# Performance work log

Measured on AMD Instinct MI355X. Metric: run time of the kernel, lower is better.

The kernel has to match this reference:

```python
import jax, jax.numpy as jnp
import numpy as np

BANDWIDTH = 8.0  # gaussian kernel std


def setup_inputs() -> dict:
    key = jax.random.key(0)
    k1, k2 = jax.random.split(key)
    B, N, M, D = 2, 8192, 8192, 64
    return {
        "points": jax.random.normal(k1, (B, N, D), dtype=jnp.float32),
        "ref_points": jax.random.normal(k2, (B, M, D), dtype=jnp.float32),
    }


def reference(points, ref_points):
    # Squared pairwise distances via the |x|^2 + |y|^2 - 2<x,y> expansion
    # (same math as ((x_i - y_j)**2).sum(-1), avoids a [B,N,M,D] intermediate).
    sq_p = jnp.sum(points * points, axis=-1)          # [B,N]
    sq_r = jnp.sum(ref_points * ref_points, axis=-1)  # [B,M]
    s_ij = (sq_p[:, :, None] + sq_r[:, None, :]
            - 2.0 * jnp.einsum('bnd,bmd->bnm', points, ref_points))  # [B,N,M]
    # Gaussian kernel
    k_ij = jnp.exp(s_ij * (-1.0 / (2.0 * BANDWIDTH ** 2)))  # [B,N,M]
    # Weighted mean of reference points (nominator.sum(2) / k_ij.sum(2))
    nominator = jnp.einsum('bnm,bmd->bnd', k_ij, ref_points)  # [B,N,D]
    denominator = jnp.sum(k_ij, axis=-1, keepdims=True)       # [B,N,1]
    return nominator / denominator
```

## Files before the change

### kernel.cpp

```cpp
#include <hip/hip_runtime.h>

constexpr int B_ = 2, N_ = 8192, M_ = 8192, Dd = 64;
constexpr int TN = 128;
constexpr int TM = 64;
constexpr int SPLIT = 8;
constexpr int MCHUNK = M_ / SPLIT;
constexpr int NCHUNKS = MCHUNK / TM;
constexpr int NT = N_ / TN;
constexpr float LOG2E   = 1.4426950408889634f;
constexpr float SCALE_S = LOG2E / 64.0f;
constexpr float SCALE_N = -LOG2E / 128.0f;

using s16x8 = __attribute__((ext_vector_type(8))) short;
using f32x4 = __attribute__((ext_vector_type(4))) float;
using f32x2v = __attribute__((ext_vector_type(2))) float;
using bf16x2 = __attribute__((ext_vector_type(2))) __bf16;

#if defined(__has_builtin)
#if __has_builtin(__builtin_amdgcn_exp2f)
#define EXP2(x) __builtin_amdgcn_exp2f(x)
#endif
#endif
#ifndef EXP2
#define EXP2(x) exp2f(x)
#endif

__device__ __forceinline__ unsigned pk2(float lo, float hi) {
  f32x2v f;
  f[0] = lo;
  f[1] = hi;
  bf16x2 h = __builtin_convertvector(f, bf16x2);
  return __builtin_bit_cast(unsigned, h);
}
__device__ __forceinline__ f32x4 mfma16(s16x8 a, s16x8 b, f32x4 c) {
  return __builtin_amdgcn_mfma_f32_16x16x32_bf16(a, b, c, 0, 0, 0);
}
__device__ __forceinline__ float dot4(float4 f) {
  return f.x * f.x + f.y * f.y + f.z * f.z + f.w * f.w;
}


__global__ __launch_bounds__(256, 4) void msflash_kernel(
    const float* __restrict__ pts, const float* __restrict__ ref,
    float* __restrict__ num_acc, float* __restrict__ den_acc) {
  __shared__ unsigned short ldsY2[2][TM][72];
  __shared__ unsigned short ldsYT2[2][Dd][64];
  __shared__ unsigned short ldsQ[4][16][32];
  __shared__ float lds_bm2[2][TM];

  const int tid  = threadIdx.x;
  const int w    = tid >> 6;
  const int lane = tid & 63;
  const int l15  = lane & 15, quad = lane >> 4;
  const int ytsw = quad + (l15 & 7);
  const int psm  = l15 & 3;

  const int s  = blockIdx.x & (SPLIT - 1);
  const int r  = blockIdx.x >> 3;
  const int bb = r / NT;
  const int nt_ = r % NT;
  const int n0 = nt_ * TN;
  const int m_begin = s * MCHUNK;

  const int rowl_s = tid >> 2, q_s = tid & 3;
  const float* ybase = ref + ((size_t)bb * M_ + m_begin + rowl_s) * Dd + q_s * 16;
  float4 fv0, fv1, fv2, fv3;

  auto loadfv = [&](int cc) {
    const float* yp = ybase + (size_t)cc * TM * Dd;
    fv0 = ((const float4*)yp)[0];
    fv1 = ((const float4*)yp)[1];
    fv2 = ((const float4*)yp)[2];
    fv3 = ((const float4*)yp)[3];
  };
  auto stage = [&](int bp) {
    unsigned pkd[8] = {pk2(fv0.x, fv0.y), pk2(fv0.z, fv0.w),
                       pk2(fv1.x, fv1.y), pk2(fv1.z, fv1.w),
                       pk2(fv2.x, fv2.y), pk2(fv2.z, fv2.w),
                       pk2(fv3.x, fv3.y), pk2(fv3.z, fv3.w)};
    float sq = dot4(fv0) + dot4(fv1) + dot4(fv2) + dot4(fv3);
    sq += __shfl_xor(sq, 1);
    sq += __shfl_xor(sq, 2);
    if (q_s == 0) lds_bm2[bp][rowl_s] = sq * SCALE_N;
    uint4* dv = (uint4*)&ldsY2[bp][rowl_s][q_s * 16];
    dv[0] = make_uint4(pkd[0], pkd[1], pkd[2], pkd[3]);
    dv[1] = make_uint4(pkd[4], pkd[5], pkd[6], pkd[7]);
    const int tsw = (rowl_s >> 3) + 2 * q_s;
    const int mlo = rowl_s & 7;
#pragma unroll
    for (int j = 0; j < 8; j++) {
      const int d0 = q_s * 16 + 2 * j;
      const int c0 = (tsw + ((2 * j) & 7)) & 7;
      const int c1 = (tsw + ((2 * j + 1) & 7)) & 7;
      ldsYT2[bp][d0][(c0 << 3) + mlo]     = (unsigned short)pkd[j];
      ldsYT2[bp][d0 + 1][(c1 << 3) + mlo] = (unsigned short)(pkd[j] >> 16);
    }
  };

  loadfv(0);
  unsigned short (*ldsX)[72] = (unsigned short (*)[72]) & ldsY2[0][0][0];
  float* lds_an2 = (float*)&ldsQ[0][0][0];
  {
    const int rowl = tid >> 1, half = tid & 1;
    const float* gp = pts + ((size_t)bb * N_ + n0 + rowl) * Dd + half * 32;
    float sq = 0.f;
    unsigned pkd[16];
#pragma unroll
    for (int i = 0; i < 8; i++) {
      float4 f = ((const float4*)gp)[i];
      sq += dot4(f);
      pkd[2 * i + 0] = pk2(f.x, f.y);
      pkd[2 * i + 1] = pk2(f.z, f.w);
    }
    sq += __shfl_xor(sq, 1);
    if (half == 0) lds_an2[rowl] = sq * SCALE_N;
    uint4* dv = (uint4*)&ldsX[rowl][half * 32];
#pragma unroll
    for (int i = 0; i < 4; i++)
      dv[i] = make_uint4(pkd[4 * i], pkd[4 * i + 1], pkd[4 * i + 2], pkd[4 * i + 3]);
  }
  __syncthreads();

  s16x8 bx[2][2];
  float anr_s[2];
#pragma unroll
  for (int rt = 0; rt < 2; rt++) {
#pragma unroll
    for (int ks = 0; ks < 2; ks++)
      bx[rt][ks] = *(const s16x8*)&ldsX[w * 32 + rt * 16 + l15][ks * 32 + quad * 8];
    anr_s[rt] = lds_an2[w * 32 + rt * 16 + l15];
  }
  __syncthreads();

  stage(0);
  loadfv(1);
  __syncthreads();

  f32x4 o[2][4], den[2];
#pragma unroll
  for (int rt = 0; rt < 2; rt++) {
    den[rt] = f32x4{0.f, 0.f, 0.f, 0.f};
#pragma unroll
    for (int dt = 0; dt < 4; dt++) o[rt][dt] = f32x4{0.f, 0.f, 0.f, 0.f};
  }
  s16x8 ones;
#pragma unroll
  for (int j = 0; j < 8; j++) ones[j] = (l15 == 0) ? (short)0x3F80 : (short)0;

  int p = 0;
  for (int c = 0; c < NCHUNKS; ++c) {
    f32x4 sf[2][4];
#pragma unroll
    for (int ct = 0; ct < 4; ct++) {
      s16x8 a0 = *(const s16x8*)&ldsY2[p][ct * 16 + l15][quad * 8];
      s16x8 a1 = *(const s16x8*)&ldsY2[p][ct * 16 + l15][32 + quad * 8];
#pragma unroll
      for (int rt = 0; rt < 2; rt++) {
        f32x4 acc = f32x4{0.f, 0.f, 0.f, 0.f};
        acc = mfma16(a0, bx[rt][0], acc);
        acc = mfma16(a1, bx[rt][1], acc);
        sf[rt][ct] = acc;
      }
    }
#pragma unroll
    for (int ks = 0; ks < 2; ks++) {
      f32x4 bmA = *(const f32x4*)&lds_bm2[p][(2 * ks + 0) * 16 + quad * 4];
      f32x4 bmB = *(const f32x4*)&lds_bm2[p][(2 * ks + 1) * 16 + quad * 4];
      s16x8 pf01[2];
#pragma unroll
      for (int rt = 0; rt < 2; rt++) {
#pragma unroll
        for (int cl = 0; cl < 2; cl++) {
          const f32x4& bm = cl ? bmB : bmA;
          const f32x4& sv = sf[rt][2 * ks + cl];
          float e0 = EXP2(sv[0] * SCALE_S + (anr_s[rt] + bm[0]));
          float e1 = EXP2(sv[1] * SCALE_S + (anr_s[rt] + bm[1]));
          float e2 = EXP2(sv[2] * SCALE_S + (anr_s[rt] + bm[2]));
          float e3 = EXP2(sv[3] * SCALE_S + (anr_s[rt] + bm[3]));
          const int ch = ((2 * cl + (quad >> 1)) ^ psm);
          *(uint2*)&ldsQ[w][l15][ch * 8 + (quad & 1) * 4] =
              make_uint2(pk2(e0, e1), pk2(e2, e3));
        }
        pf01[rt] = *(const s16x8*)&ldsQ[w][l15][(quad ^ psm) * 8];
      }
#pragma unroll
      for (int dt = 0; dt < 4; dt++) {
        const unsigned short* yt = &ldsYT2[p][dt * 16 + l15][0];
        s16x8 a = *(const s16x8*)&yt[((ytsw + 4 * ks + 2 * dt) & 7) << 3];
        o[0][dt] = mfma16(a, pf01[0], o[0][dt]);
        o[1][dt] = mfma16(a, pf01[1], o[1][dt]);
      }
      den[0] = mfma16(ones, pf01[0], den[0]);
      den[1] = mfma16(ones, pf01[1], den[1]);
    }
    stage(p ^ 1);
    loadfv(c + 2 < NCHUNKS ? c + 2 : NCHUNKS - 1);
    __syncthreads();
    p ^= 1;
  }

  float* ldsO = (float*)&ldsY2[0][0][0] + (size_t)w * 1152;
  float* nb = num_acc + ((size_t)bb * N_ + n0) * Dd;
#pragma unroll
  for (int rt = 0; rt < 2; rt++) {
#pragma unroll
    for (int dt = 0; dt < 4; dt++) {
      const int base = l15 * 66 + dt * 16 + quad * 4;
      *(float2*)&ldsO[base + 0] = make_float2(o[rt][dt][0], o[rt][dt][1]);
      *(float2*)&ldsO[base + 2] = make_float2(o[rt][dt][2], o[rt][dt][3]);
    }
    const int nrow = w * 32 + rt * 16;
#pragma unroll
    for (int rr = 0; rr < 16; rr++) {
      float v = ldsO[rr * 66 + lane];
      atomicAdd(&nb[(size_t)(nrow + rr) * Dd + lane], v);
    }
    if (quad == 0)
      atomicAdd(&den_acc[(size_t)bb * N_ + n0 + nrow + l15], den[rt][0]);
  }
}

__global__ __launch_bounds__(256) void msdiv_kernel(
    const float* __restrict__ num, const float* __restrict__ den,
    float* __restrict__ out) {
  const int i = blockIdx.x * 256 + threadIdx.x;
  float4 v = ((const float4*)num)[i];
  const float inv = 1.0f / den[i >> 4];
  ((float4*)out)[i] = make_float4(v.x * inv, v.y * inv, v.z * inv, v.w * inv);
}

extern "C" void kernel_launch(void* const* d_in, const int* in_sizes, int n_in,
                              void* d_out, int out_size, void* d_ws, size_t ws_size,
                              hipStream_t stream) {
  const float* pts = (const float*)d_in[0];
  const float* ref = (const float*)d_in[1];
  float* out = (float*)d_out;
  float* num = (float*)d_ws;
  float* den = num + (size_t)B_ * N_ * Dd;
  const size_t acc_bytes = ((size_t)B_ * N_ * Dd + (size_t)B_ * N_) * sizeof(float);

  hipMemsetAsync(d_ws, 0, acc_bytes, stream);
  msflash_kernel<<<dim3(B_ * NT * SPLIT), dim3(256), 0, stream>>>(pts, ref, num, den);
  const int tot4 = B_ * N_ * Dd / 4;
  msdiv_kernel<<<dim3(tot4 / 256), dim3(256), 0, stream>>>(num, den, out);
}
```

Before: 157.0 us.

## Switch flash mean-shift kernel to 32x32x16 MFMA with register-shuffled P fragments

Replaces the 16x16x32 bf16 MFMA tiling with 32x32x16 MFMA, so each wave computes its 32-row tile with fewer, larger matrix ops. The exp outputs are regrouped into the B-operand layout with a cross-half lane shuffle instead of a round trip through per-wave LDS scratch. The denominator is summed in scalar registers instead of by an extra ones-vector MFMA. The double-buffered LDS staging with register prefetch is dropped for a single buffer with two barriers per chunk. That cuts LDS use and may raise occupancy, but global load latency is no longer overlapped with compute.

```diff
diff --git a/kernel.cpp b/kernel.cpp
--- a/kernel.cpp
+++ b/kernel.cpp
@@ -11,8 +11,8 @@
 constexpr float SCALE_S = LOG2E / 64.0f;
 constexpr float SCALE_N = -LOG2E / 128.0f;
 
-using s16x8 = __attribute__((ext_vector_type(8))) short;
-using f32x4 = __attribute__((ext_vector_type(4))) float;
+using s16x8  = __attribute__((ext_vector_type(8))) short;
+using f32x16 = __attribute__((ext_vector_type(16))) float;
 using f32x2v = __attribute__((ext_vector_type(2))) float;
 using bf16x2 = __attribute__((ext_vector_type(2))) __bf16;
 
@@ -32,8 +32,8 @@
   bf16x2 h = __builtin_convertvector(f, bf16x2);
   return __builtin_bit_cast(unsigned, h);
 }
-__device__ __forceinline__ f32x4 mfma16(s16x8 a, s16x8 b, f32x4 c) {
-  return __builtin_amdgcn_mfma_f32_16x16x32_bf16(a, b, c, 0, 0, 0);
+__device__ __forceinline__ f32x16 mfma32(s16x8 a, s16x8 b, f32x16 c) {
+  return __builtin_amdgcn_mfma_f32_32x32x16_bf16(a, b, c, 0, 0, 0);
 }
 __device__ __forceinline__ float dot4(float4 f) {
   return f.x * f.x + f.y * f.y + f.z * f.z + f.w * f.w;
@@ -43,17 +43,17 @@
 __global__ __launch_bounds__(256, 4) void msflash_kernel(
     const float* __restrict__ pts, const float* __restrict__ ref,
     float* __restrict__ num_acc, float* __restrict__ den_acc) {
-  __shared__ unsigned short ldsY2[2][TM][72];
-  __shared__ unsigned short ldsYT2[2][Dd][64];
-  __shared__ unsigned short ldsQ[4][16][32];
-  __shared__ float lds_bm2[2][TM];
+  __shared__ __align__(16) unsigned char smem[18944];
+  unsigned short (*ldsY)[72]  = (unsigned short (*)[72])  smem;
+  unsigned short (*ldsYT)[64] = (unsigned short (*)[64]) (smem + 9216);
+  float* bm2 = (float*)(smem + 17408);
+  float* an2 = (float*)(smem + 18432);
 
   const int tid  = threadIdx.x;
   const int w    = tid >> 6;
   const int lane = tid & 63;
-  const int l15  = lane & 15, quad = lane >> 4;
-  const int ytsw = quad + (l15 & 7);
-  const int psm  = l15 & 3;
+  const int c32  = lane & 31;
+  const int hi   = lane >> 5;
 
   const int s  = blockIdx.x & (SPLIT - 1);
   const int r  = blockIdx.x >> 3;
@@ -64,25 +64,20 @@
 
   const int rowl_s = tid >> 2, q_s = tid & 3;
   const float* ybase = ref + ((size_t)bb * M_ + m_begin + rowl_s) * Dd + q_s * 16;
-  float4 fv0, fv1, fv2, fv3;
-
-  auto loadfv = [&](int cc) {
+
+  auto stage = [&](int cc) {
     const float* yp = ybase + (size_t)cc * TM * Dd;
-    fv0 = ((const float4*)yp)[0];
-    fv1 = ((const float4*)yp)[1];
-    fv2 = ((const float4*)yp)[2];
-    fv3 = ((const float4*)yp)[3];
-  };
-  auto stage = [&](int bp) {
-    unsigned pkd[8] = {pk2(fv0.x, fv0.y), pk2(fv0.z, fv0.w),
-                       pk2(fv1.x, fv1.y), pk2(fv1.z, fv1.w),
-                       pk2(fv2.x, fv2.y), pk2(fv2.z, fv2.w),
-                       pk2(fv3.x, fv3.y), pk2(fv3.z, fv3.w)};
-    float sq = dot4(fv0) + dot4(fv1) + dot4(fv2) + dot4(fv3);
+    float4 a0 = ((const float4*)yp)[0];
+    float4 a1 = ((const float4*)yp)[1];
+    float4 a2 = ((const float4*)yp)[2];
+    float4 a3 = ((const float4*)yp)[3];
+    unsigned pkd[8] = {pk2(a0.x, a0.y), pk2(a0.z, a0.w), pk2(a1.x, a1.y), pk2(a1.z, a1.w),
+                       pk2(a2.x, a2.y), pk2(a2.z, a2.w), pk2(a3.x, a3.y), pk2(a3.z, a3.w)};
+    float sq = dot4(a0) + dot4(a1) + dot4(a2) + dot4(a3);
     sq += __shfl_xor(sq, 1);
     sq += __shfl_xor(sq, 2);
-    if (q_s == 0) lds_bm2[bp][rowl_s] = sq * SCALE_N;
-    uint4* dv = (uint4*)&ldsY2[bp][rowl_s][q_s * 16];
+    if (q_s == 0) bm2[rowl_s] = sq * SCALE_N;
+    uint4* dv = (uint4*)&ldsY[rowl_s][q_s * 16];
     dv[0] = make_uint4(pkd[0], pkd[1], pkd[2], pkd[3]);
     dv[1] = make_uint4(pkd[4], pkd[5], pkd[6], pkd[7]);
     const int tsw = (rowl_s >> 3) + 2 * q_s;
@@ -92,14 +87,12 @@
       const int d0 = q_s * 16 + 2 * j;
       const int c0 = (tsw + ((2 * j) & 7)) & 7;
       const int c1 = (tsw + ((2 * j + 1) & 7)) & 7;
-      ldsYT2[bp][d0][(c0 << 3) + mlo]     = (unsigned short)pkd[j];
-      ldsYT2[bp][d0 + 1][(c1 << 3) + mlo] = (unsigned short)(pkd[j] >> 16);
+      ldsYT[d0][(c0 << 3) + mlo]     = (unsigned short)pkd[j];
+      ldsYT[d0 + 1][(c1 << 3) + mlo] = (unsigned short)(pkd[j] >> 16);
     }
   };
 
-  loadfv(0);
-  unsigned short (*ldsX)[72] = (unsigned short (*)[72]) & ldsY2[0][0][0];
-  float* lds_an2 = (float*)&ldsQ[0][0][0];
+  unsigned short (*ldsX)[72] = (unsigned short (*)[72]) smem;
   {
     const int rowl = tid >> 1, half = tid & 1;
     const float* gp = pts + ((size_t)bb * N_ + n0 + rowl) * Dd + half * 32;
@@ -113,7 +106,7 @@
       pkd[2 * i + 1] = pk2(f.z, f.w);
     }
     sq += __shfl_xor(sq, 1);
-    if (half == 0) lds_an2[rowl] = sq * SCALE_N;
+    if (half == 0) an2[rowl] = sq * SCALE_N;
     uint4* dv = (uint4*)&ldsX[rowl][half * 32];
 #pragma unroll
     for (int i = 0; i < 4; i++)
@@ -121,103 +114,87 @@
   }
   __syncthreads();
 
-  s16x8 bx[2][2];
-  float anr_s[2];
-#pragma unroll
-  for (int rt = 0; rt < 2; rt++) {
-#pragma unroll
-    for (int ks = 0; ks < 2; ks++)
-      bx[rt][ks] = *(const s16x8*)&ldsX[w * 32 + rt * 16 + l15][ks * 32 + quad * 8];
-    anr_s[rt] = lds_an2[w * 32 + rt * 16 + l15];
+  s16x8 bx[4];
+#pragma unroll
+  for (int k = 0; k < 4; k++)
+    bx[k] = *(const s16x8*)&ldsX[w * 32 + c32][k * 16 + hi * 8];
+  const float anr = an2[w * 32 + c32];
+
+  f32x16 o0, o1;
+#pragma unroll
+  for (int i = 0; i < 16; i++) { o0[i] = 0.f; o1[i] = 0.f; }
+  float dacc = 0.f;
+
+  const int ytbase = hi + 2 * (c32 >> 4) + (c32 & 7);
+
+  for (int c = 0; c < NCHUNKS; ++c) {
+    __syncthreads();
+    stage(c);
+    __syncthreads();
+
+#pragma unroll
+    for (int t = 0; t < 2; t++) {
+      f32x16 sf;
+#pragma unroll
+      for (int i = 0; i < 16; i++) sf[i] = 0.f;
+#pragma unroll
+      for (int k = 0; k < 4; k++) {
+        s16x8 a = *(const s16x8*)&ldsY[t * 32 + c32][k * 16 + hi * 8];
+        sf = mfma32(a, bx[k], sf);
+      }
+      unsigned dw[8], sw[8];
+#pragma unroll
+      for (int rg = 0; rg < 4; rg++) {
+        float4 bm = *(const float4*)&bm2[t * 32 + 8 * rg + 4 * hi];
+        float e0 = EXP2(sf[4 * rg + 0] * SCALE_S + (anr + bm.x));
+        float e1 = EXP2(sf[4 * rg + 1] * SCALE_S + (anr + bm.y));
+        float e2 = EXP2(sf[4 * rg + 2] * SCALE_S + (anr + bm.z));
+        float e3 = EXP2(sf[4 * rg + 3] * SCALE_S + (anr + bm.w));
+        dacc += (e0 + e1) + (e2 + e3);
+        dw[2 * rg + 0] = pk2(e0, e1);
+        dw[2 * rg + 1] = pk2(e2, e3);
+      }
+#pragma unroll
+      for (int j = 0; j < 8; j++) sw[j] = __shfl_xor(dw[j], 32);
+#pragma unroll
+      for (int kk = 0; kk < 2; kk++) {
+        unsigned f0 = hi ? sw[4 * kk + 2] : dw[4 * kk + 0];
+        unsigned f1 = hi ? sw[4 * kk + 3] : dw[4 * kk + 1];
+        unsigned f2 = hi ? dw[4 * kk + 2] : sw[4 * kk + 0];
+        unsigned f3 = hi ? dw[4 * kk + 3] : sw[4 * kk + 1];
+        s16x8 pf = __builtin_bit_cast(s16x8, make_uint4(f0, f1, f2, f3));
+        const int ks = 2 * t + kk;
+        const int F0 = (2 * ks + ytbase) & 7;
+        const int F1 = (2 * ks + ytbase + 4) & 7;
+        s16x8 a0 = *(const s16x8*)&ldsYT[c32][F0 * 8];
+        s16x8 a1 = *(const s16x8*)&ldsYT[32 + c32][F1 * 8];
+        o0 = mfma32(a0, pf, o0);
+        o1 = mfma32(a1, pf, o1);
+      }
+    }
   }
+
+  dacc += __shfl_xor(dacc, 32);
   __syncthreads();
-
-  stage(0);
-  loadfv(1);
-  __syncthreads();
-
-  f32x4 o[2][4], den[2];
-#pragma unroll
-  for (int rt = 0; rt < 2; rt++) {
-    den[rt] = f32x4{0.f, 0.f, 0.f, 0.f};
-#pragma unroll
-    for (int dt = 0; dt < 4; dt++) o[rt][dt] = f32x4{0.f, 0.f, 0.f, 0.f};
+  float* sc = (float*)smem + (size_t)w * 1152;
+  float* nb = num_acc + ((size_t)bb * N_ + n0 + w * 32) * Dd;
+#pragma unroll
+  for (int h = 0; h < 2; h++) {
+    const f32x16& oh = h ? o1 : o0;
+#pragma unroll
+    for (int rg = 0; rg < 4; rg++) {
+      *(float4*)&sc[c32 * 36 + 8 * rg + 4 * hi] =
+          make_float4(oh[4 * rg + 0], oh[4 * rg + 1], oh[4 * rg + 2], oh[4 * rg + 3]);
+    }
+#pragma unroll
+    for (int rr = 0; rr < 16; rr++) {
+      const int row = 2 * rr + hi;
+      float v = sc[row * 36 + c32];
+      atomicAdd(&nb[(size_t)row * Dd + h * 32 + c32], v);
+    }
   }
-  s16x8 ones;
-#pragma unroll
-  for (int j = 0; j < 8; j++) ones[j] = (l15 == 0) ? (short)0x3F80 : (short)0;
-
-  int p = 0;
-  for (int c = 0; c < NCHUNKS; ++c) {
-    f32x4 sf[2][4];
-#pragma unroll
-    for (int ct = 0; ct < 4; ct++) {
-      s16x8 a0 = *(const s16x8*)&ldsY2[p][ct * 16 + l15][quad * 8];
-      s16x8 a1 = *(const s16x8*)&ldsY2[p][ct * 16 + l15][32 + quad * 8];
-#pragma unroll
-      for (int rt = 0; rt < 2; rt++) {
-        f32x4 acc = f32x4{0.f, 0.f, 0.f, 0.f};
-        acc = mfma16(a0, bx[rt][0], acc);
-        acc = mfma16(a1, bx[rt][1], acc);
-        sf[rt][ct] = acc;
-      }
-    }
-#pragma unroll
-    for (int ks = 0; ks < 2; ks++) {
-      f32x4 bmA = *(const f32x4*)&lds_bm2[p][(2 * ks + 0) * 16 + quad * 4];
-      f32x4 bmB = *(const f32x4*)&lds_bm2[p][(2 * ks + 1) * 16 + quad * 4];
-      s16x8 pf01[2];
-#pragma unroll
-      for (int rt = 0; rt < 2; rt++) {
-#pragma unroll
-        for (int cl = 0; cl < 2; cl++) {
-          const f32x4& bm = cl ? bmB : bmA;
-          const f32x4& sv = sf[rt][2 * ks + cl];
-          float e0 = EXP2(sv[0] * SCALE_S + (anr_s[rt] + bm[0]));
-          float e1 = EXP2(sv[1] * SCALE_S + (anr_s[rt] + bm[1]));
-          float e2 = EXP2(sv[2] * SCALE_S + (anr_s[rt] + bm[2]));
-          float e3 = EXP2(sv[3] * SCALE_S + (anr_s[rt] + bm[3]));
-          const int ch = ((2 * cl + (quad >> 1)) ^ psm);
-          *(uint2*)&ldsQ[w][l15][ch * 8 + (quad & 1) * 4] =
-              make_uint2(pk2(e0, e1), pk2(e2, e3));
-        }
-        pf01[rt] = *(const s16x8*)&ldsQ[w][l15][(quad ^ psm) * 8];
-      }
-#pragma unroll
-      for (int dt = 0; dt < 4; dt++) {
-        const unsigned short* yt = &ldsYT2[p][dt * 16 + l15][0];
-        s16x8 a = *(const s16x8*)&yt[((ytsw + 4 * ks + 2 * dt) & 7) << 3];
-        o[0][dt] = mfma16(a, pf01[0], o[0][dt]);
-        o[1][dt] = mfma16(a, pf01[1], o[1][dt]);
-      }
-      den[0] = mfma16(ones, pf01[0], den[0]);
-      den[1] = mfma16(ones, pf01[1], den[1]);
-    }
-    stage(p ^ 1);
-    loadfv(c + 2 < NCHUNKS ? c + 2 : NCHUNKS - 1);
-    __syncthreads();
-    p ^= 1;
-  }
-
-  float* ldsO = (float*)&ldsY2[0][0][0] + (size_t)w * 1152;
-  float* nb = num_acc + ((size_t)bb * N_ + n0) * Dd;
-#pragma unroll
-  for (int rt = 0; rt < 2; rt++) {
-#pragma unroll
-    for (int dt = 0; dt < 4; dt++) {
-      const int base = l15 * 66 + dt * 16 + quad * 4;
-      *(float2*)&ldsO[base + 0] = make_float2(o[rt][dt][0], o[rt][dt][1]);
-      *(float2*)&ldsO[base + 2] = make_float2(o[rt][dt][2], o[rt][dt][3]);
-    }
-    const int nrow = w * 32 + rt * 16;
-#pragma unroll
-    for (int rr = 0; rr < 16; rr++) {
-      float v = ldsO[rr * 66 + lane];
-      atomicAdd(&nb[(size_t)(nrow + rr) * Dd + lane], v);
-    }
-    if (quad == 0)
-      atomicAdd(&den_acc[(size_t)bb * N_ + n0 + nrow + l15], den[rt][0]);
-  }
+  if (hi == 0)
+    atomicAdd(&den_acc[(size_t)bb * N_ + n0 + w * 32 + c32], dacc);
 }
 
 __global__ __launch_bounds__(256) void msdiv_kernel(
```

After: 129.1 us. 17.8% less time.
